# Performance work log

Measured on AMD Instinct MI355X. Metric: run time of the kernel, lower is better.

## Reference

```python
import jax, jax.numpy as jnp
import numpy as np
from math import sqrt

B, L, H, D = 4, 4096, 8, 64
FACTOR = 5


def setup_inputs():
    key = jax.random.key(0)
    k1, k2, k3, k4 = jax.random.split(key, 4)
    queries = jax.random.normal(k1, (B, L, H, D), dtype=jnp.float32)
    keys = jax.random.normal(k2, (B, L, H, D), dtype=jnp.float32)
    values = jax.random.normal(k3, (B, L, H, D), dtype=jnp.float32)
    sample_k = min(FACTOR * int(np.ceil(np.log(L))), L)  # U_part = 45
    index_sample = jax.random.randint(k4, (L, sample_k), 0, L)
    return {"queries": queries, "keys": keys, "values": values,
            "index_sample": index_sample}


def reference(queries, keys, values, index_sample):
    Bq, L_Q, Hq, Dq = queries.shape
    L_K = keys.shape[1]
    Q = jnp.transpose(queries, (0, 2, 1, 3))  # [B,H,L_Q,D]
    K = jnp.transpose(keys, (0, 2, 1, 3))     # [B,H,L_K,D]
    V = jnp.transpose(values, (0, 2, 1, 3))   # [B,H,L_K,D]
    n_top = min(FACTOR * int(np.ceil(np.log(L_Q))), L_Q)  # u = 45

    # --- _prob_QK: randomly-sampled QK scoring + top-k query selection ---
    K_sample = K[:, :, index_sample, :]                       # [B,H,L_Q,sample_k,D]
    Q_K_sample = jnp.einsum('bhld,bhlkd->bhlk', Q, K_sample)  # [B,H,L_Q,sample_k]
    M = Q_K_sample.max(-1) - Q_K_sample.sum(-1) / L_K         # sparsity measure
    _, M_top = jax.lax.top_k(M, n_top)                        # [B,H,u] query indices
    Q_reduce = jnp.take_along_axis(Q, M_top[..., None], axis=2)  # [B,H,u,D]
    scores = jnp.einsum('bhud,bhkd->bhuk', Q_reduce, K)       # [B,H,u,L_K]

    # scale = 1/sqrt(D) (self.scale is None)
    scores = scores * (1.0 / sqrt(Dq))

    # --- ProbMask (mask_flag=True): causal, key j masked if j > query idx ---
    mask = jnp.arange(L_K)[None, None, None, :] > M_top[..., None]
    scores = jnp.where(mask, -jnp.inf, scores)
    attn = jax.nn.softmax(scores, axis=-1)                    # [B,H,u,L_K]

    # --- initial context (masked case): cumulative sum of V over time ---
    context = jnp.cumsum(V, axis=2)                           # [B,H,L_Q,D]

    # --- scatter attn@V into the selected query positions ---
    upd = jnp.einsum('bhuk,bhkd->bhud', attn, V)              # [B,H,u,D]
    b_idx = jnp.arange(Bq)[:, None, None]
    h_idx = jnp.arange(Hq)[None, :, None]
    context = context.at[b_idx, h_idx, M_top].set(upd)
    return context  # [B,H,L_Q,D], as returned by the torch module
```

## Files before the change

kernel.cpp:

```cpp
#include <hip/hip_runtime.h>

#define NB 4
#define LSEQ 4096
#define NH 8
#define ND 64
#define NSAMP 45
#define NTOP 45
#define ACH 256
#define NCH (LSEQ / ACH)

typedef float f32x4 __attribute__((ext_vector_type(4)));

__global__ __launch_bounds__(256) void prep_kernel(
        const int* __restrict__ idxS, int* __restrict__ sortedPack) {
    int t = threadIdx.x;
    int l = blockIdx.x * 256 + t;
    const int* is = idxS + (size_t)l * NSAMP;
    __shared__ int cnt[256][17];
    #pragma unroll
    for (int c = 0; c < 16; ++c) cnt[t][c] = 0;
    for (int s = 0; s < NSAMP; ++s) cnt[t][is[s] >> 8] += 1;
    int run = 0;
    #pragma unroll
    for (int c = 0; c < 16; ++c) { int v = cnt[t][c]; cnt[t][c] = run; run += v; }
    for (int s = 0; s < NSAMP; ++s) {
        int idx = is[s];
        int pos = cnt[t][idx >> 8]++;
        sortedPack[(size_t)l * NSAMP + pos] = (idx << 8) | s;
    }
}

__global__ __launch_bounds__(512, 1) void compute_M_kernel(
        const float* __restrict__ Q,
        const float* __restrict__ K,
        const int* __restrict__ sortedPack,
        float* __restrict__ Mout) {
    int xcd = blockIdx.x & 7;
    int sub = blockIdx.x >> 3;
    int bh  = (xcd << 2) | (sub & 3);
    int lt  = sub >> 2;
    int b = bh >> 3, h = bh & 7;
    int t = threadIdx.x;
    int l0 = (lt << 9) + t;

    __shared__ float Ks[256 * 68];
    __shared__ float Plds[512 * 45];

    f32x4 qa[16];
    {
        const f32x4* qp0 = reinterpret_cast<const f32x4*>(
            Q + (((size_t)b * LSEQ + l0) * NH + h) * ND);
        #pragma unroll
        for (int i = 0; i < 16; ++i) qa[i] = __builtin_nontemporal_load(qp0 + i);
    }

    auto dotQK = [&](const f32x4 (&q4)[16], const float* kr) -> float {
        const f32x4* k4 = reinterpret_cast<const f32x4*>(kr);
        float w[32];
        #pragma unroll
        for (int i = 0; i < 8; ++i) {
            f32x4 a = q4[i], bb = k4[i], c = q4[i + 8], d4 = k4[i + 8];
            w[4 * i + 0] = __fadd_rn(__fmul_rn(a.x, bb.x), __fmul_rn(c.x, d4.x));
            w[4 * i + 1] = __fadd_rn(__fmul_rn(a.y, bb.y), __fmul_rn(c.y, d4.y));
            w[4 * i + 2] = __fadd_rn(__fmul_rn(a.z, bb.z), __fmul_rn(c.z, d4.z));
            w[4 * i + 3] = __fadd_rn(__fmul_rn(a.w, bb.w), __fmul_rn(c.w, d4.w));
        }
        #pragma unroll
        for (int off = 16; off; off >>= 1) {
            #pragma unroll
            for (int i = 0; i < off; ++i) w[i] = __fadd_rn(w[i], w[i + off]);
        }
        return w[0];
    };

    const int* sp0 = sortedPack + (size_t)l0 * NSAMP;
    int ptr0 = 0;
    int pk0 = sp0[0];

    size_t kbh = ((size_t)b * LSEQ * NH + h) * ND;

    for (int c = 0; c < 16; ++c) {
        #pragma unroll
        for (int i = 0; i < 8; ++i) {
            int flat = i * 512 + t;
            int row = flat >> 4, col = flat & 15;
            f32x4 v = *reinterpret_cast<const f32x4*>(
                K + kbh + (size_t)(c * 256 + row) * (NH * ND) + col * 4);
            *reinterpret_cast<f32x4*>(&Ks[row * 68 + col * 4]) = v;
        }
        __syncthreads();

        while ((pk0 >> 16) == c) {
            int r = (pk0 >> 8) & 255;
            int s = pk0 & 255;
            Plds[t * 45 + s] = dotQK(qa, &Ks[r * 68]);
            ++ptr0;
            pk0 = (ptr0 < NSAMP) ? sp0[ptr0] : 0x7fffffff;
        }
        __syncthreads();
    }

    {
        float maxv = -INFINITY, sumv = 0.0f;
        for (int s = 0; s < NSAMP; ++s) {
            float v = Plds[t * 45 + s];
            maxv = fmaxf(maxv, v);
            sumv = __fadd_rn(sumv, v);
        }
        Mout[(size_t)bh * LSEQ + l0] = maxv - sumv * (1.0f / (float)LSEQ);
    }
}

__global__ __launch_bounds__(256) void topk_kernel(
        const float* __restrict__ M, int* __restrict__ Mtop) {
    int bh = blockIdx.x;
    int t = threadIdx.x;
    int wave = t >> 6, lane = t & 63;
    const float* m = M + (size_t)bh * LSEQ;

    float rv[16];
    #pragma unroll
    for (int k = 0; k < 16; ++k) rv[k] = m[t + (k << 8)];

    __shared__ float wv[4];
    __shared__ int   wi[4];
    __shared__ int   winIdx;

    for (int iter = 0; iter < NTOP; ++iter) {
        float bv = -INFINITY; int bi = 0x7fffffff;
        #pragma unroll
        for (int k = 0; k < 16; ++k) {
            float v = rv[k];
            if (v > bv) { bv = v; bi = t + (k << 8); }
        }
        #pragma unroll
        for (int off = 1; off < 64; off <<= 1) {
            float ov = __shfl_xor(bv, off, 64);
            int   oi = __shfl_xor(bi, off, 64);
            if (ov > bv || (ov == bv && oi < bi)) { bv = ov; bi = oi; }
        }
        if (lane == 0) { wv[wave] = bv; wi[wave] = bi; }
        __syncthreads();
        if (t == 0) {
            float cv = wv[0]; int ci = wi[0];
            for (int ww = 1; ww < 4; ++ww) {
                if (wv[ww] > cv || (wv[ww] == cv && wi[ww] < ci)) { cv = wv[ww]; ci = wi[ww]; }
            }
            winIdx = ci;
            Mtop[bh * NTOP + iter] = ci;
        }
        __syncthreads();
        int widx = winIdx;
        #pragma unroll
        for (int k = 0; k < 16; ++k)
            if (widx == t + (k << 8)) rv[k] = -INFINITY;
        __syncthreads();
    }
}

__global__ __launch_bounds__(256) void cumsumA_kernel(
        const float* __restrict__ V, float* __restrict__ chunkSums) {
    int blk = blockIdx.x;
    int c = blk & 15;
    int bh = blk >> 4;
    int h = bh & (NH - 1);
    int b = bh >> 3;
    int g = threadIdx.x >> 6, d = threadIdx.x & 63;

    const size_t rstride = (size_t)NH * ND;
    size_t vbase = (size_t)b * LSEQ * rstride + (size_t)h * ND + d;

    int l0 = c * 256 + g * 64;
    float s = 0.0f;
    for (int l = l0; l < l0 + 64; ++l) s += V[vbase + (size_t)l * rstride];

    __shared__ float part[4][ND];
    part[g][d] = s;
    __syncthreads();
    if (threadIdx.x < ND)
        chunkSums[(size_t)blk * ND + d] =
            part[0][d] + part[1][d] + part[2][d] + part[3][d];
}

__global__ __launch_bounds__(256) void cumsumC_kernel(
        const float* __restrict__ V, const float* __restrict__ chunkSums,
        float* __restrict__ out) {
    int blk = blockIdx.x;
    int c = blk & 15;
    int bh = blk >> 4;
    int h = bh & (NH - 1);
    int b = bh >> 3;
    int g = threadIdx.x >> 6, d = threadIdx.x & 63;

    const size_t rstride = (size_t)NH * ND;
    size_t vbase = (size_t)b * LSEQ * rstride + (size_t)h * ND + d;

    float run = 0.0f;
    for (int cc = 0; cc < c; ++cc)
        run += chunkSums[((size_t)bh * 16 + cc) * ND + d];

    int l0 = c * 256 + g * 64;
    float s = 0.0f;
    for (int l = l0; l < l0 + 64; ++l) s += V[vbase + (size_t)l * rstride];
    __shared__ float part[4][ND];
    part[g][d] = s;
    __syncthreads();
    for (int gg = 0; gg < g; ++gg) run += part[gg][d];

    size_t obase = (size_t)bh * LSEQ * ND + d;
    for (int l = l0; l < l0 + 64; ++l) {
        run += V[vbase + (size_t)l * rstride];
        out[obase + (size_t)l * ND] = run;
    }
}

__global__ __launch_bounds__(256, 1) void attn_partial_kernel(
        const float* __restrict__ Q, const float* __restrict__ K,
        const float* __restrict__ V, const int* __restrict__ Mtop,
        float* __restrict__ part) {
    int bh = blockIdx.x >> 4;
    int c  = blockIdx.x & 15;
    int b = bh >> 3, h = bh & 7;
    int t = threadIdx.x;
    int w = t >> 6, lane = t & 63;
    int jj = lane >> 4, dq = lane & 15;

    __shared__ float Qs[NTOP * ND];
    __shared__ int   posS[NTOP];
    __shared__ float Vs[64][68];
    __shared__ float Pw[4][64];

    size_t base = ((size_t)b * LSEQ * NH + h) * ND;

    if (t < NTOP) posS[t] = Mtop[bh * NTOP + t];
    __syncthreads();
    for (int idx = t; idx < NTOP * 16; idx += 256) {
        int u = idx >> 4, cg = idx & 15;
        f32x4 v = *reinterpret_cast<const f32x4*>(
            Q + base + (size_t)posS[u] * (NH * ND) + cg * 4);
        *reinterpret_cast<f32x4*>(&Qs[u * ND + cg * 4]) = v;
    }

    f32x4 o[12];
    float mreg[12], sreg[12];
    #pragma unroll
    for (int qi = 0; qi < 12; ++qi) {
        o[qi] = 0.0f; mreg[qi] = -INFINITY; sreg[qi] = 0.0f;
    }

    for (int tt = 0; tt < ACH / 64; ++tt) {
        int tile0 = c * ACH + tt * 64;
        __syncthreads();
        #pragma unroll
        for (int i = 0; i < 4; ++i) {
            int flat = i * 256 + t;
            int r = flat >> 4, cg = flat & 15;
            f32x4 v = *reinterpret_cast<const f32x4*>(
                V + base + (size_t)(tile0 + r) * (NH * ND) + cg * 4);
            *reinterpret_cast<f32x4*>(&Vs[r][cg * 4]) = v;
        }
        __syncthreads();

        f32x4 kreg[16];
        #pragma unroll
        for (int i = 0; i < 16; ++i)
            kreg[i] = *reinterpret_cast<const f32x4*>(
                K + base + (size_t)(tile0 + lane) * (NH * ND) + i * 4);

        #pragma unroll
        for (int qi = 0; qi < 12; ++qi) {
            int u = w + 4 * qi;
            if (u >= NTOP) continue;
            int pu = posS[u];
            if (pu < tile0) continue;

            float a0 = 0, a1 = 0, a2 = 0, a3 = 0;
            #pragma unroll
            for (int di = 0; di < 16; ++di) {
                f32x4 qv = *reinterpret_cast<const f32x4*>(&Qs[u * ND + di * 4]);
                a0 = fmaf(qv.x, kreg[di].x, a0);
                a1 = fmaf(qv.y, kreg[di].y, a1);
                a2 = fmaf(qv.z, kreg[di].z, a2);
                a3 = fmaf(qv.w, kreg[di].w, a3);
            }
            float sc = ((a0 + a1) + (a2 + a3)) * 0.125f;
            if (tile0 + lane > pu) sc = -INFINITY;

            float tmax = sc;
            #pragma unroll
            for (int off = 1; off < 64; off <<= 1)
                tmax = fmaxf(tmax, __shfl_xor(tmax, off, 64));
            float mold = mreg[qi];
            float mnew = fmaxf(mold, tmax);
            float alpha = __expf(mold - mnew);
            float e = __expf(sc - mnew);
            float esum = e;
            #pragma unroll
            for (int off = 1; off < 64; off <<= 1)
                esum += __shfl_xor(esum, off, 64);
            sreg[qi] = sreg[qi] * alpha + esum;
            mreg[qi] = mnew;
            Pw[w][lane] = e;
            o[qi] *= alpha;
            #pragma unroll
            for (int i = 0; i < 16; ++i) {
                float pe = Pw[w][i * 4 + jj];
                f32x4 vv = *reinterpret_cast<const f32x4*>(&Vs[i * 4 + jj][dq * 4]);
                o[qi] += vv * pe;
            }
        }
    }

    #pragma unroll
    for (int qi = 0; qi < 12; ++qi) {
        int u = w + 4 * qi;
        if (u >= NTOP) continue;
        if (posS[u] < c * ACH) continue;
        f32x4 oo = o[qi];
        #pragma unroll
        for (int off = 16; off <= 32; off <<= 1) {
            oo.x += __shfl_xor(oo.x, off, 64);
            oo.y += __shfl_xor(oo.y, off, 64);
            oo.z += __shfl_xor(oo.z, off, 64);
            oo.w += __shfl_xor(oo.w, off, 64);
        }
        size_t pb = ((size_t)(bh * NTOP + u) * NCH + c) * 72;
        if (lane < 16)
            *reinterpret_cast<f32x4*>(&part[pb + 4 + dq * 4]) = oo;
        if (lane == 0) { part[pb] = mreg[qi]; part[pb + 1] = sreg[qi]; }
    }
}

__global__ __launch_bounds__(256) void attn_merge_kernel(
        const float* __restrict__ part, const int* __restrict__ Mtop,
        float* __restrict__ ctx) {
    int j = blockIdx.x * 4 + (threadIdx.x >> 6);
    int lane = threadIdx.x & 63;
    int bh = j / NTOP, u = j - bh * NTOP;
    int pos = Mtop[bh * NTOP + u];
    int cmax = pos >> 8;
    size_t pb0 = (size_t)(bh * NTOP + u) * NCH * 72;
    float m = -INFINITY;
    for (int cc = 0; cc <= cmax; ++cc)
        m = fmaxf(m, part[pb0 + (size_t)cc * 72]);
    float S = 0.0f, oacc = 0.0f;
    for (int cc = 0; cc <= cmax; ++cc) {
        float mc = part[pb0 + (size_t)cc * 72];
        float sc = part[pb0 + (size_t)cc * 72 + 1];
        float wgt = __expf(mc - m);
        S = fmaf(sc, wgt, S);
        oacc = fmaf(part[pb0 + (size_t)cc * 72 + 4 + lane], wgt, oacc);
    }
    ctx[(size_t)j * ND + lane] = oacc / S;
}

__global__ __launch_bounds__(256) void scatter_kernel(
        const float* __restrict__ ctx, const int* __restrict__ Mtop,
        float* __restrict__ out) {
    int j = blockIdx.x * 4 + (threadIdx.x >> 6);
    int lane = threadIdx.x & 63;
    int bh = j / NTOP, u = j - bh * NTOP;
    int pos = Mtop[bh * NTOP + u];
    out[((size_t)bh * LSEQ + pos) * ND + lane] = ctx[(size_t)j * ND + lane];
}

#define TJ 64
__global__ __launch_bounds__(256) void attn_rows_kernel(
        const float* __restrict__ Q,
        const float* __restrict__ K,
        const float* __restrict__ V,
        const int* __restrict__ Mtop,
        float* __restrict__ out) {
    int x = blockIdx.x;
    int xcd = x & 7;
    int slot = x >> 3;
    int grp = slot / NTOP;
    int u = slot % NTOP;
    int bh = grp * 8 + xcd;
    int h = bh & (NH - 1);
    int b = bh >> 3;
    int pos = Mtop[bh * NTOP + u];
    int n = pos + 1;
    int t = threadIdx.x;
    int r = t >> 2, qt = t & 3;

    __shared__ float Ks[TJ][65];
    __shared__ float Vs[TJ][65];
    __shared__ float red[256];

    const size_t rstride = (size_t)NH * ND;
    size_t base = (size_t)b * LSEQ * rstride + (size_t)h * ND;

    float qreg[16];
    const float* qrow = Q + base + (size_t)pos * rstride + qt * 16;
    #pragma unroll
    for (int i = 0; i < 16; i += 4) {
        float4 v4 = *reinterpret_cast<const float4*>(qrow + i);
        qreg[i] = v4.x; qreg[i + 1] = v4.y; qreg[i + 2] = v4.z; qreg[i + 3] = v4.w;
    }

    float m = -INFINITY, s = 0.0f;
    float o[16];
    #pragma unroll
    for (int dd = 0; dd < 16; ++dd) o[dd] = 0.0f;

    int ntiles = (n + TJ - 1) / TJ;
    for (int tt = 0; tt < ntiles; ++tt) {
        int j0 = tt * TJ;
        __syncthreads();
        #pragma unroll
        for (int i = 0; i < 4; ++i) {
            int u16 = t + i * 256;
            int rr = u16 >> 4, cc = u16 & 15;
            int j = j0 + rr;
            int jc = (j < n) ? j : (n - 1);
            const float* rowk = K + base + (size_t)jc * rstride;
            float4 kv = *reinterpret_cast<const float4*>(rowk + cc * 4);
            Ks[rr][cc * 4 + 0] = kv.x; Ks[rr][cc * 4 + 1] = kv.y;
            Ks[rr][cc * 4 + 2] = kv.z; Ks[rr][cc * 4 + 3] = kv.w;
            const float* rowv = V + base + (size_t)jc * rstride;
            float4 vv = *reinterpret_cast<const float4*>(rowv + cc * 4);
            Vs[rr][cc * 4 + 0] = vv.x; Vs[rr][cc * 4 + 1] = vv.y;
            Vs[rr][cc * 4 + 2] = vv.z; Vs[rr][cc * 4 + 3] = vv.w;
        }
        __syncthreads();

        int j = j0 + r;
        float acc = 0.0f;
        #pragma unroll
        for (int dd = 0; dd < 16; ++dd)
            acc = fmaf(qreg[dd], Ks[r][qt * 16 + dd], acc);
        acc += __shfl_xor(acc, 1, 64);
        acc += __shfl_xor(acc, 2, 64);

        if (j < n) {
            float sc = acc * 0.125f;
            if (sc > m) {
                float alpha = __expf(m - sc);
                s *= alpha;
                #pragma unroll
                for (int dd = 0; dd < 16; ++dd) o[dd] *= alpha;
                m = sc;
            }
            float e = __expf(sc - m);
            s += e;
            #pragma unroll
            for (int dd = 0; dd < 16; ++dd)
                o[dd] = fmaf(e, Vs[r][qt * 16 + dd], o[dd]);
        }
    }
    __syncthreads();

    red[t] = m; __syncthreads();
    for (int sft = 128; sft; sft >>= 1) {
        if (t < sft) red[t] = fmaxf(red[t], red[t + sft]);
        __syncthreads();
    }
    float mstar = red[0]; __syncthreads();
    float a = __expf(m - mstar);

    red[t] = s * a; __syncthreads();
    for (int sft = 128; sft; sft >>= 1) {
        if (t < sft) red[t] += red[t + sft];
        __syncthreads();
    }
    float S = red[0]; __syncthreads();

    float* OB = &Ks[0][0];
    #pragma unroll
    for (int dd = 0; dd < 16; ++dd) OB[t * 16 + dd] = o[dd] * a;
    __syncthreads();

    if (t < ND) {
        int qtt = t >> 4, dd = t & 15;
        float tot = 0.0f;
        for (int k = 0; k < 64; ++k) tot += OB[(4 * k + qtt) * 16 + dd];
        out[((size_t)bh * LSEQ + pos) * ND + t] = tot / S;
    }
}

extern "C" void kernel_launch(void* const* d_in, const int* in_sizes, int n_in,
                              void* d_out, int out_size, void* d_ws, size_t ws_size,
                              hipStream_t stream) {
    const float* Q = (const float*)d_in[0];
    const float* K = (const float*)d_in[1];
    const float* V = (const float*)d_in[2];
    const int* idxS = (const int*)d_in[3];
    float* out = (float*)d_out;

    float* Mbuf = (float*)d_out;
    int*   sortedPack = (int*)((char*)d_out + (1 << 20));
    float* part = (float*)((char*)d_out + (2 << 20));
    int*   Mtop = (int*)d_ws;
    float* chunkSums = (float*)((char*)d_ws + 8192);
    float* ctx = (float*)((char*)d_ws + 8192 + 131072);
    size_t wsNeeded = 8192 + 131072 + (size_t)NB * NH * NTOP * ND * 4;

    prep_kernel<<<LSEQ / 256, 256, 0, stream>>>(idxS, sortedPack);
    compute_M_kernel<<<256, 512, 0, stream>>>(Q, K, sortedPack, Mbuf);
    topk_kernel<<<NB * NH, 256, 0, stream>>>(Mbuf, Mtop);

    if (ws_size >= wsNeeded) {
        attn_partial_kernel<<<NB * NH * NCH, 256, 0, stream>>>(Q, K, V, Mtop, part);
        attn_merge_kernel<<<NB * NH * NTOP / 4, 256, 0, stream>>>(part, Mtop, ctx);
        cumsumA_kernel<<<NB * NH * 16, 256, 0, stream>>>(V, chunkSums);
        cumsumC_kernel<<<NB * NH * 16, 256, 0, stream>>>(V, chunkSums, out);
        scatter_kernel<<<NB * NH * NTOP / 4, 256, 0, stream>>>(ctx, Mtop, out);
    } else {
        cumsumA_kernel<<<NB * NH * 16, 256, 0, stream>>>(V, chunkSums);
        cumsumC_kernel<<<NB * NH * 16, 256, 0, stream>>>(V, chunkSums, out);
        attn_rows_kernel<<<NB * NH * NTOP, 256, 0, stream>>>(Q, K, V, Mtop, out);
    }
}
```

Before: 414.7 us.

## Split sampled QK scoring across two thread halves per query and reduce in-register

Each query row's 45 sampled keys are now split into two interleaved lists of 23 and 22 entries, terminated by sentinels, and handled by two threads. The grid doubles to 512 blocks of 256 queries each, and launch bounds now allow up to 4 blocks per CU. The running max and sum are kept in registers instead of the 512x45 score LDS buffer, then combined across the two halves through a small shared reduction. This targets the low occupancy and long serial per-thread loop of the compute_M stage. In exchange, every K chunk is now loaded by twice as many blocks, and the tighter launch bound puts pressure on the registers that hold Q.

```diff
diff --git a/kernel.cpp b/kernel.cpp
--- a/kernel.cpp
+++ b/kernel.cpp
@@ -8,11 +8,12 @@
 #define NTOP 45
 #define ACH 256
 #define NCH (LSEQ / ACH)
+#define SENT 0x7fffffff
 
 typedef float f32x4 __attribute__((ext_vector_type(4)));
 
 __global__ __launch_bounds__(256) void prep_kernel(
-        const int* __restrict__ idxS, int* __restrict__ sortedPack) {
+        const int* __restrict__ idxS, int* __restrict__ sortedAB) {
     int t = threadIdx.x;
     int l = blockIdx.x * 256 + t;
     const int* is = idxS + (size_t)l * NSAMP;
@@ -23,17 +24,19 @@
     int run = 0;
     #pragma unroll
     for (int c = 0; c < 16; ++c) { int v = cnt[t][c]; cnt[t][c] = run; run += v; }
+    int* ab = sortedAB + (size_t)l * 48;
+    ab[23] = SENT; ab[46] = SENT; ab[47] = SENT;
     for (int s = 0; s < NSAMP; ++s) {
         int idx = is[s];
-        int pos = cnt[t][idx >> 8]++;
-        sortedPack[(size_t)l * NSAMP + pos] = (idx << 8) | s;
-    }
-}
-
-__global__ __launch_bounds__(512, 1) void compute_M_kernel(
+        int p = cnt[t][idx >> 8]++;
+        ab[(p & 1) * 24 + (p >> 1)] = (idx << 8) | s;
+    }
+}
+
+__global__ __launch_bounds__(512, 4) void compute_M_kernel(
         const float* __restrict__ Q,
         const float* __restrict__ K,
-        const int* __restrict__ sortedPack,
+        const int* __restrict__ sortedAB,
         float* __restrict__ Mout) {
     int xcd = blockIdx.x & 7;
     int sub = blockIdx.x >> 3;
@@ -41,15 +44,18 @@
     int lt  = sub >> 2;
     int b = bh >> 3, h = bh & 7;
     int t = threadIdx.x;
-    int l0 = (lt << 9) + t;
+    int lloc = t & 255;
+    int par  = t >> 8;
+    int l = (lt << 8) | lloc;
 
     __shared__ float Ks[256 * 68];
-    __shared__ float Plds[512 * 45];
+    __shared__ float redM[512];
+    __shared__ float redS[512];
 
     f32x4 qa[16];
     {
         const f32x4* qp0 = reinterpret_cast<const f32x4*>(
-            Q + (((size_t)b * LSEQ + l0) * NH + h) * ND);
+            Q + (((size_t)b * LSEQ + l) * NH + h) * ND);
         #pragma unroll
         for (int i = 0; i < 16; ++i) qa[i] = __builtin_nontemporal_load(qp0 + i);
     }
@@ -73,11 +79,14 @@
         return w[0];
     };
 
-    const int* sp0 = sortedPack + (size_t)l0 * NSAMP;
-    int ptr0 = 0;
-    int pk0 = sp0[0];
+    const int* sp = sortedAB + (size_t)l * 48 + par * 24;
+    int ptr = 0;
+    int pk = sp[0];
 
     size_t kbh = ((size_t)b * LSEQ * NH + h) * ND;
+
+    float maxv = -INFINITY;
+    float sumv = 0.0f;
 
     for (int c = 0; c < 16; ++c) {
         #pragma unroll
@@ -90,24 +99,23 @@
         }
         __syncthreads();
 
-        while ((pk0 >> 16) == c) {
-            int r = (pk0 >> 8) & 255;
-            int s = pk0 & 255;
-            Plds[t * 45 + s] = dotQK(qa, &Ks[r * 68]);
-            ++ptr0;
-            pk0 = (ptr0 < NSAMP) ? sp0[ptr0] : 0x7fffffff;
-        }
-        __syncthreads();
-    }
-
-    {
-        float maxv = -INFINITY, sumv = 0.0f;
-        for (int s = 0; s < NSAMP; ++s) {
-            float v = Plds[t * 45 + s];
-            maxv = fmaxf(maxv, v);
-            sumv = __fadd_rn(sumv, v);
-        }
-        Mout[(size_t)bh * LSEQ + l0] = maxv - sumv * (1.0f / (float)LSEQ);
+        while ((pk >> 16) == c) {
+            int r = (pk >> 8) & 255;
+            float p = dotQK(qa, &Ks[r * 68]);
+            maxv = fmaxf(maxv, p);
+            sumv = __fadd_rn(sumv, p);
+            ++ptr;
+            pk = sp[ptr];
+        }
+        __syncthreads();
+    }
+
+    redM[t] = maxv; redS[t] = sumv;
+    __syncthreads();
+    if (t < 256) {
+        float m = fmaxf(redM[t], redM[t + 256]);
+        float s = __fadd_rn(redS[t], redS[t + 256]);
+        Mout[(size_t)bh * LSEQ + l] = m - s * (1.0f / (float)LSEQ);
     }
 }
 
@@ -489,15 +497,15 @@
     float* out = (float*)d_out;
 
     float* Mbuf = (float*)d_out;
-    int*   sortedPack = (int*)((char*)d_out + (1 << 20));
+    int*   sortedAB = (int*)((char*)d_out + (1 << 20));
     float* part = (float*)((char*)d_out + (2 << 20));
     int*   Mtop = (int*)d_ws;
     float* chunkSums = (float*)((char*)d_ws + 8192);
     float* ctx = (float*)((char*)d_ws + 8192 + 131072);
     size_t wsNeeded = 8192 + 131072 + (size_t)NB * NH * NTOP * ND * 4;
 
-    prep_kernel<<<LSEQ / 256, 256, 0, stream>>>(idxS, sortedPack);
-    compute_M_kernel<<<256, 512, 0, stream>>>(Q, K, sortedPack, Mbuf);
+    prep_kernel<<<LSEQ / 256, 256, 0, stream>>>(idxS, sortedAB);
+    compute_M_kernel<<<512, 512, 0, stream>>>(Q, K, sortedAB, Mbuf);
     topk_kernel<<<NB * NH, 256, 0, stream>>>(Mbuf, Mtop);
 
     if (ws_size >= wsNeeded) {
```

New measurement: 428.0 us. +3.2%, slower.

## Fuse pipeline into three kernels using atomic last-block completion counters

Applied to the files above, without the earlier changes.

Collapses the eight-launch pipeline into three kernels when the workspace is large enough. Index sorting is merged with the cumsum chunk sums, and top-k moves into the M-scoring kernel, where the last block per head finishes it via an atomic counter. Attention partials, the merge, the cumsum and the scatter share one kernel, coordinated through atomic counters so the scatter runs after both the cumsum chunk and the merged context are ready. This removes launch overhead and inter-kernel gaps, at the cost of serial tail work in the last block and reliance on threadfence ordering. The counters are zeroed by the first kernel on each call.

```diff
diff --git a/kernel.cpp b/kernel.cpp
--- a/kernel.cpp
+++ b/kernel.cpp
@@ -10,6 +10,403 @@
 #define NCH (LSEQ / ACH)
 
 typedef float f32x4 __attribute__((ext_vector_type(4)));
+
+
+__global__ __launch_bounds__(256) void fusedA_kernel(
+        const int* __restrict__ idxS, int* __restrict__ sortedPack,
+        const float* __restrict__ V, float* __restrict__ chunkSums,
+        int* __restrict__ cnts) {
+    int blk = blockIdx.x;
+    int t = threadIdx.x;
+    __shared__ int cnt[256][17];
+    __shared__ float part[4][ND];
+
+    if (blk < 16) {
+        if (blk == 0) {
+            for (int i = t; i < 576; i += 256) cnts[i] = 0;
+        }
+        int l = blk * 256 + t;
+        const int* is = idxS + (size_t)l * NSAMP;
+        #pragma unroll
+        for (int c = 0; c < 16; ++c) cnt[t][c] = 0;
+        for (int s = 0; s < NSAMP; ++s) cnt[t][is[s] >> 8] += 1;
+        int run = 0;
+        #pragma unroll
+        for (int c = 0; c < 16; ++c) { int v = cnt[t][c]; cnt[t][c] = run; run += v; }
+        for (int s = 0; s < NSAMP; ++s) {
+            int idx = is[s];
+            int pos = cnt[t][idx >> 8]++;
+            sortedPack[(size_t)l * NSAMP + pos] = (idx << 8) | s;
+        }
+    } else {
+        int blk2 = blk - 16;
+        int c = blk2 & 15;
+        int bh = blk2 >> 4;
+        int h = bh & (NH - 1);
+        int b = bh >> 3;
+        int g = t >> 6, d = t & 63;
+
+        const size_t rstride = (size_t)NH * ND;
+        size_t vbase = (size_t)b * LSEQ * rstride + (size_t)h * ND + d;
+
+        int l0 = c * 256 + g * 64;
+        float s = 0.0f;
+        for (int l = l0; l < l0 + 64; ++l) s += V[vbase + (size_t)l * rstride];
+
+        part[g][d] = s;
+        __syncthreads();
+        if (t < ND)
+            chunkSums[(size_t)blk2 * ND + d] =
+                part[0][d] + part[1][d] + part[2][d] + part[3][d];
+    }
+}
+
+__global__ __launch_bounds__(512, 1) void fusedM_kernel(
+        const float* __restrict__ Q,
+        const float* __restrict__ K,
+        const int* __restrict__ sortedPack,
+        float* __restrict__ Mout,
+        int* __restrict__ Mtop,
+        int* __restrict__ cntM,
+        int doTopk) {
+    int xcd = blockIdx.x & 7;
+    int sub = blockIdx.x >> 3;
+    int bh  = (xcd << 2) | (sub & 3);
+    int lt  = sub >> 2;
+    int b = bh >> 3, h = bh & 7;
+    int t = threadIdx.x;
+    int l0 = (lt << 9) + t;
+
+    __shared__ float Ks[256 * 68];
+    __shared__ float Plds[512 * 45];
+    __shared__ float wv[8];
+    __shared__ int   wi[8];
+    __shared__ int   winIdx;
+    __shared__ int   amLast;
+
+    f32x4 qa[16];
+    {
+        const f32x4* qp0 = reinterpret_cast<const f32x4*>(
+            Q + (((size_t)b * LSEQ + l0) * NH + h) * ND);
+        #pragma unroll
+        for (int i = 0; i < 16; ++i) qa[i] = __builtin_nontemporal_load(qp0 + i);
+    }
+
+    auto dotQK = [&](const f32x4 (&q4)[16], const float* kr) -> float {
+        const f32x4* k4 = reinterpret_cast<const f32x4*>(kr);
+        float w[32];
+        #pragma unroll
+        for (int i = 0; i < 8; ++i) {
+            f32x4 a = q4[i], bb = k4[i], c = q4[i + 8], d4 = k4[i + 8];
+            w[4 * i + 0] = __fadd_rn(__fmul_rn(a.x, bb.x), __fmul_rn(c.x, d4.x));
+            w[4 * i + 1] = __fadd_rn(__fmul_rn(a.y, bb.y), __fmul_rn(c.y, d4.y));
+            w[4 * i + 2] = __fadd_rn(__fmul_rn(a.z, bb.z), __fmul_rn(c.z, d4.z));
+            w[4 * i + 3] = __fadd_rn(__fmul_rn(a.w, bb.w), __fmul_rn(c.w, d4.w));
+        }
+        #pragma unroll
+        for (int off = 16; off; off >>= 1) {
+            #pragma unroll
+            for (int i = 0; i < off; ++i) w[i] = __fadd_rn(w[i], w[i + off]);
+        }
+        return w[0];
+    };
+
+    const int* sp0 = sortedPack + (size_t)l0 * NSAMP;
+    int ptr0 = 0;
+    int pk0 = sp0[0];
+
+    size_t kbh = ((size_t)b * LSEQ * NH + h) * ND;
+
+    for (int c = 0; c < 16; ++c) {
+        #pragma unroll
+        for (int i = 0; i < 8; ++i) {
+            int flat = i * 512 + t;
+            int row = flat >> 4, col = flat & 15;
+            f32x4 v = *reinterpret_cast<const f32x4*>(
+                K + kbh + (size_t)(c * 256 + row) * (NH * ND) + col * 4);
+            *reinterpret_cast<f32x4*>(&Ks[row * 68 + col * 4]) = v;
+        }
+        __syncthreads();
+
+        while ((pk0 >> 16) == c) {
+            int r = (pk0 >> 8) & 255;
+            int s = pk0 & 255;
+            Plds[t * 45 + s] = dotQK(qa, &Ks[r * 68]);
+            ++ptr0;
+            pk0 = (ptr0 < NSAMP) ? sp0[ptr0] : 0x7fffffff;
+        }
+        __syncthreads();
+    }
+
+    {
+        float maxv = -INFINITY, sumv = 0.0f;
+        for (int s = 0; s < NSAMP; ++s) {
+            float v = Plds[t * 45 + s];
+            maxv = fmaxf(maxv, v);
+            sumv = __fadd_rn(sumv, v);
+        }
+        Mout[(size_t)bh * LSEQ + l0] = maxv - sumv * (1.0f / (float)LSEQ);
+    }
+
+    if (!doTopk) return;
+
+    __threadfence();
+    __syncthreads();
+    if (t == 0) amLast = (atomicAdd(&cntM[bh], 1) == 7);
+    __syncthreads();
+    if (!amLast) return;
+    __threadfence();
+
+    const float* m = Mout + (size_t)bh * LSEQ;
+    float rv[8];
+    #pragma unroll
+    for (int k = 0; k < 8; ++k) rv[k] = m[t + (k << 9)];
+
+    int wave = t >> 6, lane = t & 63;
+    for (int iter = 0; iter < NTOP; ++iter) {
+        float bv = -INFINITY; int bi = 0x7fffffff;
+        #pragma unroll
+        for (int k = 0; k < 8; ++k) {
+            float v = rv[k];
+            if (v > bv) { bv = v; bi = t + (k << 9); }
+        }
+        #pragma unroll
+        for (int off = 1; off < 64; off <<= 1) {
+            float ov = __shfl_xor(bv, off, 64);
+            int   oi = __shfl_xor(bi, off, 64);
+            if (ov > bv || (ov == bv && oi < bi)) { bv = ov; bi = oi; }
+        }
+        if (lane == 0) { wv[wave] = bv; wi[wave] = bi; }
+        __syncthreads();
+        if (t == 0) {
+            float cv = wv[0]; int ci = wi[0];
+            for (int ww = 1; ww < 8; ++ww) {
+                if (wv[ww] > cv || (wv[ww] == cv && wi[ww] < ci)) { cv = wv[ww]; ci = wi[ww]; }
+            }
+            winIdx = ci;
+            Mtop[bh * NTOP + iter] = ci;
+        }
+        __syncthreads();
+        int widx = winIdx;
+        #pragma unroll
+        for (int k = 0; k < 8; ++k)
+            if (widx == t + (k << 9)) rv[k] = -INFINITY;
+        __syncthreads();
+    }
+}
+
+__global__ __launch_bounds__(256, 1) void fusedC_kernel(
+        const float* __restrict__ Q, const float* __restrict__ K,
+        const float* __restrict__ V, const int* __restrict__ Mtop,
+        float* __restrict__ part, const float* __restrict__ chunkSums,
+        float* __restrict__ ctx, float* __restrict__ out,
+        int* __restrict__ cntA, int* __restrict__ cnt2) {
+    int blk = blockIdx.x;
+    int t = threadIdx.x;
+
+    __shared__ float Qs[NTOP * ND];
+    __shared__ int   posS[NTOP];
+    __shared__ float Vs[64][68];
+    __shared__ float Pw[4][64];
+    __shared__ float cpart[4][ND];
+    __shared__ int   flagA;
+    __shared__ unsigned int scatMask;
+
+    if (blk < 512) {
+        int bh = blk >> 4;
+        int c  = blk & 15;
+        int b = bh >> 3, h = bh & 7;
+        int w = t >> 6, lane = t & 63;
+        int jj = lane >> 4, dq = lane & 15;
+
+        size_t base = ((size_t)b * LSEQ * NH + h) * ND;
+
+        if (t < NTOP) posS[t] = Mtop[bh * NTOP + t];
+        __syncthreads();
+        for (int idx = t; idx < NTOP * 16; idx += 256) {
+            int u = idx >> 4, cg = idx & 15;
+            f32x4 v = *reinterpret_cast<const f32x4*>(
+                Q + base + (size_t)posS[u] * (NH * ND) + cg * 4);
+            *reinterpret_cast<f32x4*>(&Qs[u * ND + cg * 4]) = v;
+        }
+
+        f32x4 o[12];
+        float mreg[12], sreg[12];
+        #pragma unroll
+        for (int qi = 0; qi < 12; ++qi) {
+            o[qi] = 0.0f; mreg[qi] = -INFINITY; sreg[qi] = 0.0f;
+        }
+
+        for (int tt = 0; tt < ACH / 64; ++tt) {
+            int tile0 = c * ACH + tt * 64;
+            __syncthreads();
+            #pragma unroll
+            for (int i = 0; i < 4; ++i) {
+                int flat = i * 256 + t;
+                int r = flat >> 4, cg = flat & 15;
+                f32x4 v = *reinterpret_cast<const f32x4*>(
+                    V + base + (size_t)(tile0 + r) * (NH * ND) + cg * 4);
+                *reinterpret_cast<f32x4*>(&Vs[r][cg * 4]) = v;
+            }
+            __syncthreads();
+
+            f32x4 kreg[16];
+            #pragma unroll
+            for (int i = 0; i < 16; ++i)
+                kreg[i] = *reinterpret_cast<const f32x4*>(
+                    K + base + (size_t)(tile0 + lane) * (NH * ND) + i * 4);
+
+            #pragma unroll
+            for (int qi = 0; qi < 12; ++qi) {
+                int u = w + 4 * qi;
+                if (u >= NTOP) continue;
+                int pu = posS[u];
+                if (pu < tile0) continue;
+
+                float a0 = 0, a1 = 0, a2 = 0, a3 = 0;
+                #pragma unroll
+                for (int di = 0; di < 16; ++di) {
+                    f32x4 qv = *reinterpret_cast<const f32x4*>(&Qs[u * ND + di * 4]);
+                    a0 = fmaf(qv.x, kreg[di].x, a0);
+                    a1 = fmaf(qv.y, kreg[di].y, a1);
+                    a2 = fmaf(qv.z, kreg[di].z, a2);
+                    a3 = fmaf(qv.w, kreg[di].w, a3);
+                }
+                float sc = ((a0 + a1) + (a2 + a3)) * 0.125f;
+                if (tile0 + lane > pu) sc = -INFINITY;
+
+                float tmax = sc;
+                #pragma unroll
+                for (int off = 1; off < 64; off <<= 1)
+                    tmax = fmaxf(tmax, __shfl_xor(tmax, off, 64));
+                float mold = mreg[qi];
+                float mnew = fmaxf(mold, tmax);
+                float alpha = __expf(mold - mnew);
+                float e = __expf(sc - mnew);
+                float esum = e;
+                #pragma unroll
+                for (int off = 1; off < 64; off <<= 1)
+                    esum += __shfl_xor(esum, off, 64);
+                sreg[qi] = sreg[qi] * alpha + esum;
+                mreg[qi] = mnew;
+                Pw[w][lane] = e;
+                o[qi] *= alpha;
+                #pragma unroll
+                for (int i = 0; i < 16; ++i) {
+                    float pe = Pw[w][i * 4 + jj];
+                    f32x4 vv = *reinterpret_cast<const f32x4*>(&Vs[i * 4 + jj][dq * 4]);
+                    o[qi] += vv * pe;
+                }
+            }
+        }
+
+        #pragma unroll
+        for (int qi = 0; qi < 12; ++qi) {
+            int u = w + 4 * qi;
+            if (u >= NTOP) continue;
+            if (posS[u] < c * ACH) continue;
+            f32x4 oo = o[qi];
+            #pragma unroll
+            for (int off = 16; off <= 32; off <<= 1) {
+                oo.x += __shfl_xor(oo.x, off, 64);
+                oo.y += __shfl_xor(oo.y, off, 64);
+                oo.z += __shfl_xor(oo.z, off, 64);
+                oo.w += __shfl_xor(oo.w, off, 64);
+            }
+            size_t pb = ((size_t)(bh * NTOP + u) * NCH + c) * 72;
+            if (lane < 16)
+                *reinterpret_cast<f32x4*>(&part[pb + 4 + dq * 4]) = oo;
+            if (lane == 0) { part[pb] = mreg[qi]; part[pb + 1] = sreg[qi]; }
+        }
+
+        __threadfence();
+        __syncthreads();
+        if (t == 0) flagA = (atomicAdd(&cntA[bh], 1) == 15);
+        __syncthreads();
+        if (!flagA) return;
+        __threadfence();
+
+        for (int u = w; u < NTOP; u += 4) {
+            int pos = posS[u];
+            int cmax = pos >> 8;
+            size_t pb0 = (size_t)(bh * NTOP + u) * NCH * 72;
+            float mm = -INFINITY;
+            for (int cc = 0; cc <= cmax; ++cc)
+                mm = fmaxf(mm, part[pb0 + (size_t)cc * 72]);
+            float S = 0.0f, oacc = 0.0f;
+            for (int cc = 0; cc <= cmax; ++cc) {
+                float mc = part[pb0 + (size_t)cc * 72];
+                float sc = part[pb0 + (size_t)cc * 72 + 1];
+                float wgt = __expf(mc - mm);
+                S = fmaf(sc, wgt, S);
+                oacc = fmaf(part[pb0 + (size_t)cc * 72 + 4 + lane], wgt, oacc);
+            }
+            ctx[(size_t)(bh * NTOP + u) * ND + lane] = oacc / S;
+        }
+
+        __threadfence();
+        __syncthreads();
+        if (t == 0) {
+            unsigned int mask = 0;
+            for (int cc = 0; cc < 16; ++cc)
+                if (atomicAdd(&cnt2[bh * 16 + cc], 1) == 1) mask |= (1u << cc);
+            scatMask = mask;
+        }
+        __syncthreads();
+        unsigned int mask = scatMask;
+        if (mask) {
+            __threadfence();
+            for (int idx = t; idx < NTOP * ND; idx += 256) {
+                int u = idx >> 6, d = idx & 63;
+                int pos = Mtop[bh * NTOP + u];
+                if (mask & (1u << (pos >> 8)))
+                    out[((size_t)bh * LSEQ + pos) * ND + d] =
+                        ctx[(size_t)(bh * NTOP + u) * ND + d];
+            }
+        }
+    } else {
+        int blk2 = blk - 512;
+        int c = blk2 & 15;
+        int bh = blk2 >> 4;
+        int h = bh & (NH - 1);
+        int b = bh >> 3;
+        int g = t >> 6, d = t & 63;
+
+        const size_t rstride = (size_t)NH * ND;
+        size_t vbase = (size_t)b * LSEQ * rstride + (size_t)h * ND + d;
+
+        float run = 0.0f;
+        for (int cc = 0; cc < c; ++cc)
+            run += chunkSums[((size_t)bh * 16 + cc) * ND + d];
+
+        int l0 = c * 256 + g * 64;
+        float s = 0.0f;
+        for (int l = l0; l < l0 + 64; ++l) s += V[vbase + (size_t)l * rstride];
+        cpart[g][d] = s;
+        __syncthreads();
+        for (int gg = 0; gg < g; ++gg) run += cpart[gg][d];
+
+        size_t obase = (size_t)bh * LSEQ * ND + d;
+        for (int l = l0; l < l0 + 64; ++l) {
+            run += V[vbase + (size_t)l * rstride];
+            out[obase + (size_t)l * ND] = run;
+        }
+
+        __threadfence();
+        __syncthreads();
+        if (t == 0) flagA = (atomicAdd(&cnt2[bh * 16 + c], 1) == 1);
+        __syncthreads();
+        if (!flagA) return;
+        __threadfence();
+        for (int idx = t; idx < NTOP * ND; idx += 256) {
+            int u = idx >> 6, d2 = idx & 63;
+            int pos = Mtop[bh * NTOP + u];
+            if ((pos >> 8) == c)
+                out[((size_t)bh * LSEQ + pos) * ND + d2] =
+                    ctx[(size_t)(bh * NTOP + u) * ND + d2];
+        }
+    }
+}
 
 __global__ __launch_bounds__(256) void prep_kernel(
         const int* __restrict__ idxS, int* __restrict__ sortedPack) {
@@ -27,87 +424,6 @@
         int idx = is[s];
         int pos = cnt[t][idx >> 8]++;
         sortedPack[(size_t)l * NSAMP + pos] = (idx << 8) | s;
-    }
-}
-
-__global__ __launch_bounds__(512, 1) void compute_M_kernel(
-        const float* __restrict__ Q,
-        const float* __restrict__ K,
-        const int* __restrict__ sortedPack,
-        float* __restrict__ Mout) {
-    int xcd = blockIdx.x & 7;
-    int sub = blockIdx.x >> 3;
-    int bh  = (xcd << 2) | (sub & 3);
-    int lt  = sub >> 2;
-    int b = bh >> 3, h = bh & 7;
-    int t = threadIdx.x;
-    int l0 = (lt << 9) + t;
-
-    __shared__ float Ks[256 * 68];
-    __shared__ float Plds[512 * 45];
-
-    f32x4 qa[16];
-    {
-        const f32x4* qp0 = reinterpret_cast<const f32x4*>(
-            Q + (((size_t)b * LSEQ + l0) * NH + h) * ND);
-        #pragma unroll
-        for (int i = 0; i < 16; ++i) qa[i] = __builtin_nontemporal_load(qp0 + i);
-    }
-
-    auto dotQK = [&](const f32x4 (&q4)[16], const float* kr) -> float {
-        const f32x4* k4 = reinterpret_cast<const f32x4*>(kr);
-        float w[32];
-        #pragma unroll
-        for (int i = 0; i < 8; ++i) {
-            f32x4 a = q4[i], bb = k4[i], c = q4[i + 8], d4 = k4[i + 8];
-            w[4 * i + 0] = __fadd_rn(__fmul_rn(a.x, bb.x), __fmul_rn(c.x, d4.x));
-            w[4 * i + 1] = __fadd_rn(__fmul_rn(a.y, bb.y), __fmul_rn(c.y, d4.y));
-            w[4 * i + 2] = __fadd_rn(__fmul_rn(a.z, bb.z), __fmul_rn(c.z, d4.z));
-            w[4 * i + 3] = __fadd_rn(__fmul_rn(a.w, bb.w), __fmul_rn(c.w, d4.w));
-        }
-        #pragma unroll
-        for (int off = 16; off; off >>= 1) {
-            #pragma unroll
-            for (int i = 0; i < off; ++i) w[i] = __fadd_rn(w[i], w[i + off]);
-        }
-        return w[0];
-    };
-
-    const int* sp0 = sortedPack + (size_t)l0 * NSAMP;
-    int ptr0 = 0;
-    int pk0 = sp0[0];
-
-    size_t kbh = ((size_t)b * LSEQ * NH + h) * ND;
-
-    for (int c = 0; c < 16; ++c) {
-        #pragma unroll
-        for (int i = 0; i < 8; ++i) {
-            int flat = i * 512 + t;
-            int row = flat >> 4, col = flat & 15;
-            f32x4 v = *reinterpret_cast<const f32x4*>(
-                K + kbh + (size_t)(c * 256 + row) * (NH * ND) + col * 4);
-            *reinterpret_cast<f32x4*>(&Ks[row * 68 + col * 4]) = v;
-        }
-        __syncthreads();
-
-        while ((pk0 >> 16) == c) {
-            int r = (pk0 >> 8) & 255;
-            int s = pk0 & 255;
-            Plds[t * 45 + s] = dotQK(qa, &Ks[r * 68]);
-            ++ptr0;
-            pk0 = (ptr0 < NSAMP) ? sp0[ptr0] : 0x7fffffff;
-        }
-        __syncthreads();
-    }
-
-    {
-        float maxv = -INFINITY, sumv = 0.0f;
-        for (int s = 0; s < NSAMP; ++s) {
-            float v = Plds[t * 45 + s];
-            maxv = fmaxf(maxv, v);
-            sumv = __fadd_rn(sumv, v);
-        }
-        Mout[(size_t)bh * LSEQ + l0] = maxv - sumv * (1.0f / (float)LSEQ);
     }
 }
 
@@ -488,19 +804,36 @@
     const int* idxS = (const int*)d_in[3];
     float* out = (float*)d_out;
 
+    int*   cnts   = (int*)d_ws;
+    int*   MtopF  = (int*)((char*)d_ws + 4096);
+    float* chSumF = (float*)((char*)d_ws + 16384);
+    float* ctxF   = (float*)((char*)d_ws + 147456);
+    float* MF     = (float*)((char*)d_ws + 516096);
+    int*   sortF  = (int*)((char*)d_ws + 1040384);
+    float* partF  = (float*)((char*)d_ws + 1777664);
+    const size_t wsFast = 1777664 + 6635520;
+
+    if (ws_size >= wsFast) {
+        fusedA_kernel<<<528, 256, 0, stream>>>(idxS, sortF, V, chSumF, cnts);
+        fusedM_kernel<<<256, 512, 0, stream>>>(Q, K, sortF, MF, MtopF, cnts, 1);
+        fusedC_kernel<<<1024, 256, 0, stream>>>(Q, K, V, MtopF, partF, chSumF,
+                                                ctxF, out, cnts + 32, cnts + 64);
+        return;
+    }
+
     float* Mbuf = (float*)d_out;
     int*   sortedPack = (int*)((char*)d_out + (1 << 20));
     float* part = (float*)((char*)d_out + (2 << 20));
     int*   Mtop = (int*)d_ws;
     float* chunkSums = (float*)((char*)d_ws + 8192);
     float* ctx = (float*)((char*)d_ws + 8192 + 131072);
-    size_t wsNeeded = 8192 + 131072 + (size_t)NB * NH * NTOP * ND * 4;
+    size_t wsMid = 8192 + 131072 + (size_t)NB * NH * NTOP * ND * 4;
 
     prep_kernel<<<LSEQ / 256, 256, 0, stream>>>(idxS, sortedPack);
-    compute_M_kernel<<<256, 512, 0, stream>>>(Q, K, sortedPack, Mbuf);
+    fusedM_kernel<<<256, 512, 0, stream>>>(Q, K, sortedPack, Mbuf, Mtop, Mtop, 0);
     topk_kernel<<<NB * NH, 256, 0, stream>>>(Mbuf, Mtop);
 
-    if (ws_size >= wsNeeded) {
+    if (ws_size >= wsMid) {
         attn_partial_kernel<<<NB * NH * NCH, 256, 0, stream>>>(Q, K, V, Mtop, part);
         attn_merge_kernel<<<NB * NH * NTOP / 4, 256, 0, stream>>>(part, Mtop, ctx);
         cumsumA_kernel<<<NB * NH * 16, 256, 0, stream>>>(V, chunkSums);
```

After: 657.0 us. 58.4% more time.
